# Kernel tuning notes

Measured on AMD Instinct MI355X. Metric: run time of the kernel, lower is better.

## Reference

```python
import jax, jax.numpy as jnp
import numpy as np

NPOINT, RADIUS, SIGMA, K = 1024, 0.1, 0.05, 32
KDE_K = 128  # N_points default of kernel_density_estimation_ball


def setup_inputs() -> dict:
    key = jax.random.key(0)
    ks = jax.random.split(key, 9)
    B, N, C = 4, 4096, 16

    def glorot(k, shape):
        fan_in, fan_out = shape
        return jax.random.normal(k, shape, jnp.float32) * jnp.sqrt(2.0 / (fan_in + fan_out))

    return {
        'xyz': jax.random.uniform(ks[0], (B, N, 3), jnp.float32),      # unit cube
        'feature': jax.random.normal(ks[1], (B, N, C), jnp.float32),
        'w_mlp0': glorot(ks[2], (3 + C, 128)),
        'w_mlp1': glorot(ks[3], (128, 128)),
        'w_mlp2': glorot(ks[4], (128, 256)),
        'w_wn': glorot(ks[5], (3, 32)),
        'w_nl0': glorot(ks[6], (1, 16)),
        'w_nl1': glorot(ks[7], (16, 1)),
        'w_np': glorot(ks[8], (32, 256)),
    }


def _pdist2(a, b):
    # squared pairwise distances [B, M, N]
    return (jnp.sum(a * a, -1)[:, :, None] + jnp.sum(b * b, -1)[:, None, :]
            - 2.0 * jnp.einsum('bmd,bnd->bmn', a, b))


def _fps(xyz, npoint):
    # farthest point sampling, seeded at index 0 (matches CUDA op semantics)
    B, N, _ = xyz.shape

    def step(carry, _):
        min_d, last = carry
        p = jnp.take_along_axis(xyz, last[:, None, None], axis=1)  # [B,1,3]
        d = jnp.sum((xyz - p) ** 2, -1)                            # [B,N]
        min_d = jnp.minimum(min_d, d)
        nxt = jnp.argmax(min_d, axis=1).astype(jnp.int32)
        return (min_d, nxt), nxt

    init = (jnp.full((B, N), jnp.inf, xyz.dtype), jnp.zeros((B,), jnp.int32))
    _, rest = jax.lax.scan(step, init, None, length=npoint - 1)
    return jnp.concatenate([jnp.zeros((B, 1), jnp.int32), rest.T], axis=1)  # [B,npoint]


def _ball_query(xyz, radius, k):
    # first-k-in-index-order neighbors with d2 < r^2, padded with first hit
    B, N, _ = xyz.shape
    d2 = _pdist2(xyz, xyz)
    in_ball = d2 < radius * radius                 # self always included
    j = jnp.arange(N, dtype=jnp.int32)
    keys = jnp.where(in_ball, j, j + N)            # in-ball indices sort first
    _, idx = jax.lax.top_k(-keys, k)               # k smallest keys -> positions j
    cnt = jnp.minimum(jnp.sum(in_ball, axis=-1), k)            # [B,N]
    valid = jnp.arange(k) < cnt[..., None]
    idx = jnp.where(valid, idx, idx[..., :1])
    return idx, cnt


def _kde_ball(xyz, radius, sigma, kde_k):
    idx, cnt = _ball_query(xyz, radius, kde_k)     # [B,N,kde_k], [B,N]
    b_ix = jnp.arange(xyz.shape[0])[:, None, None]
    g = xyz[b_ix, idx] - xyz[:, :, None, :]        # [B,N,kde_k,3]
    R = jnp.sqrt(jnp.float32(sigma))
    quad = jnp.sum(jnp.square(g / R), axis=-1)     # [B,N,kde_k]
    mvn = jnp.exp(-0.5 * quad - 3.0 * jnp.log(R) - 1.5 * jnp.log(2.0 * 3.1415926))
    first = mvn[..., :1]
    total = jnp.sum(mvn, axis=-1, keepdims=True)
    cntf = cnt.astype(xyz.dtype)[..., None]
    total = total - first * (jnp.float32(kde_k) - cntf)  # remove padded duplicates
    return total / cntf                             # [B,N,1]


def _knn(k, src, q):
    d2 = _pdist2(q, src)                            # [B,P,N]
    _, idx = jax.lax.top_k(-d2, k)                  # ascending distance
    return idx


def _forward(xyz, feature, w_mlp0, w_mlp1, w_mlp2, w_wn, w_nl0, w_nl1, w_np):
    B = xyz.shape[0]
    conv = lambda x, w: jax.nn.relu(jnp.einsum('bpkc,cf->bpkf', x, w))  # bias-free 1x1 conv

    fps_idx = _fps(xyz, NPOINT)
    new_xyz = jnp.take_along_axis(xyz, fps_idx[..., None], axis=1)      # [B,P,3]

    knn_idx = _knn(K, xyz, new_xyz)                                      # [B,P,K]
    b_ix = jnp.arange(B)[:, None, None]
    grouped_xyz = xyz[b_ix, knn_idx] - new_xyz[:, :, None, :]            # [B,P,K,3]
    grouped_feature = jnp.concatenate([grouped_xyz, feature[b_ix, knn_idx]], axis=-1)

    inv_density = 1.0 / _kde_ball(xyz, RADIUS, SIGMA, KDE_K)             # [B,N,1]
    grouped_density = inv_density[b_ix, knn_idx]                          # [B,P,K,1]
    density_scale = grouped_density / jnp.max(grouped_density, axis=2, keepdims=True)

    h = conv(conv(conv(grouped_feature, w_mlp0), w_mlp1), w_mlp2)        # [B,P,K,256]
    weight = conv(grouped_xyz, w_wn)                                      # [B,P,K,32]
    density_scale = conv(conv(density_scale, w_nl0), w_nl1)               # [B,P,K,1]

    pts = h * density_scale
    pts = jnp.einsum('bpkc,bpkw->bpcw', pts, weight)                      # [B,P,256,32]
    # np_conv: 1x1 kernel with stride [1, mlp[-1]] + VALID -> only c=0 slice survives
    out = jax.nn.relu(jnp.einsum('bpw,wf->bpf', pts[:, :, 0, :], w_np))   # [B,P,256]
    return new_xyz, out


def reference(xyz, feature, w_mlp0, w_mlp1, w_mlp2, w_wn, w_nl0, w_nl1, w_np):
    return _forward(xyz, feature, w_mlp0, w_mlp1, w_mlp2, w_wn, w_nl0, w_nl1, w_np)
```

## Files before the change

kernel.cpp:

```cpp
#include <hip/hip_runtime.h>
#include <math.h>

#pragma clang fp contract(off)

typedef float v2f __attribute__((ext_vector_type(2)));

__device__ __forceinline__ v2f pk_fma(v2f a, v2f b, v2f c) {
    v2f d;
    asm("v_pk_fma_f32 %0, %1, %2, %3" : "=v"(d) : "v"(a), "v"(b), "v"(c));
    return d;
}

__global__ __launch_bounds__(256) void prep_kernel(
    const float* __restrict__ xyz, const float* __restrict__ w0,
    const float* __restrict__ w1, const float* __restrict__ w2,
    float* __restrict__ norms, float* __restrict__ W1T,
    float* __restrict__ W2c)
{
    int t = blockIdx.x * 256 + threadIdx.x;
    if (t < 16384) {
        float x = xyz[t*3+0], y = xyz[t*3+1], z = xyz[t*3+2];
        norms[t] = (x*x + y*y) + z*z;
        int c = t >> 7, k = t & 127;
        W1T[c*128 + k] = w1[k*128 + c];
    }
    if (t < 128)  { W2c[t] = w2[t*256]; }
}

template<int CTRL>
__device__ __forceinline__ double dpp_f64(double v) {
    int lo = __double2loint(v), hi = __double2hiint(v);
    int plo = __builtin_amdgcn_update_dpp(lo, lo, CTRL, 0xF, 0xF, false);
    int phi = __builtin_amdgcn_update_dpp(hi, hi, CTRL, 0xF, 0xF, false);
    return __hiloint2double(phi, plo);
}
template<int CTRL>
__device__ __forceinline__ double max_f64_dpp(double k) {
    return fmax(dpp_f64<CTRL>(k), k);
}
#define KD(md2bits_f, ipi) __hiloint2double(__float_as_int(md2bits_f), (int)(ipi))

__global__ __launch_bounds__(512) void fps_kde_kernel(
    const float* __restrict__ xyz, const float* __restrict__ norms,
    float* __restrict__ new_xyz, float* __restrict__ invden)
{
    __shared__ float4 pts[4096];
    __shared__ float  nxb[3072];
    __shared__ __attribute__((aligned(16))) double swkd[2][4];
    int tid = threadIdx.x;

    if (blockIdx.x < 4) {
        int b = blockIdx.x;
        const float* Xb = xyz + b*12288;
        for (int t = tid; t < 4096; t += 512)
            pts[t] = make_float4(Xb[t*3+0], Xb[t*3+1], Xb[t*3+2], 0.0f);
        __syncthreads();
        if (tid < 256) {
            int lane = tid & 63, wave = tid >> 6;
            v2f Xp[8], Yp[8], Zp[8], md2[8];
            unsigned ip[16];
#pragma unroll
            for (int k = 0; k < 8; ++k) {
                float4 A = pts[(2*k)*256 + tid];
                float4 B = pts[(2*k+1)*256 + tid];
                Xp[k].x = A.x;  Xp[k].y = B.x;
                Yp[k].x = A.y;  Yp[k].y = B.y;
                Zp[k].x = A.z;  Zp[k].y = B.z;
                md2[k].x = INFINITY; md2[k].y = INFINITY;
                ip[2*k]   = ~((unsigned)((2*k)*256 + tid));
                ip[2*k+1] = ~((unsigned)((2*k+1)*256 + tid));
            }
            float cx = pts[0].x, cy = pts[0].y, cz = pts[0].z;
            if (tid == 0) { nxb[0] = cx; nxb[1] = cy; nxb[2] = cz; }
            int buf = 0;
            for (int it = 1; it < 1024; ++it) {
                v2f cx2, cy2, cz2;
                cx2.x = cx; cx2.y = cx;
                cy2.x = cy; cy2.y = cy;
                cz2.x = cz; cz2.y = cz;
#pragma unroll
                for (int k = 0; k < 8; ++k) {
                    v2f dx = Xp[k] - cx2, dy = Yp[k] - cy2, dz = Zp[k] - cz2;
                    v2f dd = (dx*dx + dy*dy) + dz*dz;
                    md2[k] = __builtin_elementwise_min(md2[k], dd);
                }
                double t0 = fmax(fmax(KD(md2[0].x,ip[0]),  KD(md2[0].y,ip[1])),
                                 fmax(KD(md2[1].x,ip[2]),  KD(md2[1].y,ip[3])));
                double t1 = fmax(fmax(KD(md2[2].x,ip[4]),  KD(md2[2].y,ip[5])),
                                 fmax(KD(md2[3].x,ip[6]),  KD(md2[3].y,ip[7])));
                double t2 = fmax(fmax(KD(md2[4].x,ip[8]),  KD(md2[4].y,ip[9])),
                                 fmax(KD(md2[5].x,ip[10]), KD(md2[5].y,ip[11])));
                double t3 = fmax(fmax(KD(md2[6].x,ip[12]), KD(md2[6].y,ip[13])),
                                 fmax(KD(md2[7].x,ip[14]), KD(md2[7].y,ip[15])));
                double key = fmax(fmax(t0, t1), fmax(t2, t3));
                key = max_f64_dpp<0xB1>(key);
                key = max_f64_dpp<0x4E>(key);
                key = max_f64_dpp<0x141>(key);
                key = max_f64_dpp<0x140>(key);
                key = max_f64_dpp<0x142>(key);
                key = max_f64_dpp<0x143>(key);
                if (lane == 63) swkd[buf][wave] = key;
                __syncthreads();
                double2 wab = *((const double2*)&swkd[buf][0]);
                double2 wcd = *((const double2*)&swkd[buf][2]);
                double kk = fmax(fmax(wab.x, wab.y), fmax(wcd.x, wcd.y));
                int fp = (int)(~((unsigned)__double2loint(kk)));
                float4 c = pts[fp];
                cx = c.x; cy = c.y; cz = c.z;
                if (tid == 0) { nxb[it*3+0] = cx; nxb[it*3+1] = cy; nxb[it*3+2] = cz; }
                buf ^= 1;
            }
        } else {
            for (int it = 1; it < 1024; ++it) __syncthreads();
        }
        __syncthreads();
        float* NX = new_xyz + b*3072;
        for (int t = tid; t < 3072; t += 512) NX[t] = nxb[t];
    } else {
        int idx = blockIdx.x - 4;
        int b = idx >> 9;
        int wave = tid >> 6, lane = tid & 63;
        int i_local = ((idx & 511) << 3) + wave;
        const float* Xb = xyz + b*12288;
        const float* Nb = norms + b*4096;
        for (int t = tid; t < 4096; t += 512)
            pts[t] = make_float4(Xb[t*3+0], Xb[t*3+1], Xb[t*3+2], Nb[t]);
        __syncthreads();
        float4 c = pts[i_local];
        const float Rv    = sqrtf(0.05f);
        const float inv_s = 1.0f / (Rv*Rv);
        const float K1    = -3.0f*logf(Rv) - 1.5f*logf(2.0f*3.1415926f);
        float csum = 0.0f; int cnt = 0;
        for (int j = lane; j < 4096; j += 64) {
            float4 q = pts[j];
            float dot = (c.x*q.x + c.y*q.y) + c.z*q.z;
            float t2 = 2.0f * dot;
            float d2 = (c.w + q.w) - t2;
            if (d2 < 0.01f) {
                float gx = q.x - c.x, gy = q.y - c.y, gz = q.z - c.z;
                float dd = (gx*gx + gy*gy) + gz*gz;
                csum += expf(-0.5f * (dd * inv_s) + K1);
                cnt  += 1;
            }
        }
#pragma unroll
        for (int m = 1; m < 64; m <<= 1) {
            csum += __shfl_xor(csum, m, 64);
            cnt  += __shfl_xor(cnt,  m, 64);
        }
        if (lane == 0) {
            float den = csum / (float)cnt;
            invden[b*4096 + i_local] = 1.0f / den;
        }
    }
}

__global__ __launch_bounds__(256) void knn_kernel(
    const float* __restrict__ xyz, const float* __restrict__ norms,
    const float* __restrict__ new_xyz, int* __restrict__ knn_idx)
{
    __shared__ unsigned sd2[4*4096];
    __shared__ int sIdx[4*32];
    int wave = threadIdx.x >> 6, lane = threadIdx.x & 63;
    int qg = blockIdx.x*4 + wave;
    int b = qg >> 10;
    const float* Q = new_xyz + qg*3;
    float qx = Q[0], qy = Q[1], qz = Q[2];
    float nq = (qx*qx + qy*qy) + qz*qz;
    const float* Xb = xyz + b*12288;
    const float* Nb = norms + b*4096;
    unsigned* d2w = sd2 + wave*4096;
    for (int j = lane; j < 4096; j += 64) {
        float x = Xb[j*3+0], y = Xb[j*3+1], z = Xb[j*3+2];
        float dot = (qx*x + qy*y) + qz*z;
        float t2 = 2.0f*dot;
        float d = (nq + Nb[j]) - t2;
        unsigned u = __float_as_uint(d);
        unsigned m = ((unsigned)((int)u >> 31)) | 0x80000000u;
        d2w[j] = u ^ m;
    }
    for (int r = 0; r < 32; ++r) {
        double a0 = -INFINITY, a1 = -INFINITY, a2 = -INFINITY, a3 = -INFINITY;
#pragma unroll
        for (int t = 0; t < 16; ++t) {
            int jb = t*256 + lane*4;
            uint4 v = *((const uint4*)(d2w + jb));
            a0 = fmax(a0, __hiloint2double((int)v.x, jb));
            a1 = fmax(a1, __hiloint2double((int)v.y, jb+1));
            a2 = fmax(a2, __hiloint2double((int)v.z, jb+2));
            a3 = fmax(a3, __hiloint2double((int)v.w, jb+3));
        }
        double key = fmax(fmax(a0, a1), fmax(a2, a3));
        key = max_f64_dpp<0xB1>(key);
        key = max_f64_dpp<0x4E>(key);
        key = max_f64_dpp<0x141>(key);
        key = max_f64_dpp<0x140>(key);
        key = max_f64_dpp<0x142>(key);
        key = max_f64_dpp<0x143>(key);
        int jwin = __builtin_amdgcn_readlane(__double2loint(key), 63);
        if (lane == 0) { sIdx[wave*32 + r] = jwin; d2w[jwin] = 0xFFFFFFFFu; }
    }
    if (lane < 32) knn_idx[qg*32 + lane] = sIdx[wave*32 + lane];
}

__global__ __launch_bounds__(256, 2) void group_mlp_kernel(
    const float* __restrict__ xyz, const float* __restrict__ feat,
    const float* __restrict__ new_xyz, const int* __restrict__ knn_idx,
    const float* __restrict__ invden,
    const float* __restrict__ w0, const float* __restrict__ W1T,
    const float* __restrict__ W2c, const float* __restrict__ wwn,
    const float* __restrict__ wnl0, const float* __restrict__ wnl1,
    float* __restrict__ ptsw)
{
    __shared__ float sW1[16384];
    {
        const float4* g4 = (const float4*)W1T;
        float4* s4 = (float4*)sW1;
#pragma unroll
        for (int i = 0; i < 16; ++i)
            s4[i*256 + threadIdx.x] = g4[i*256 + threadIdx.x];
    }

    int row = blockIdx.x*256 + threadIdx.x;
    int k  = row & 31;
    int pg = row >> 5;
    int b  = row >> 15;
    int j  = knn_idx[row];
    const float* Xb = xyz + b*12288;
    const float* Q  = new_xyz + pg*3;
    float in[19];
    in[0] = Xb[j*3+0] - Q[0];
    in[1] = Xb[j*3+1] - Q[1];
    in[2] = Xb[j*3+2] - Q[2];
    const float4* F = (const float4*)(feat + (size_t)(b*4096 + j)*16);
    float4 f0 = F[0], f1 = F[1], f2 = F[2], f3 = F[3];
    in[3]=f0.x; in[4]=f0.y; in[5]=f0.z; in[6]=f0.w;
    in[7]=f1.x; in[8]=f1.y; in[9]=f1.z; in[10]=f1.w;
    in[11]=f2.x; in[12]=f2.y; in[13]=f2.z; in[14]=f2.w;
    in[15]=f3.x; in[16]=f3.y; in[17]=f3.z; in[18]=f3.w;

    float gd = invden[b*4096 + j];
    float mx = gd;
#pragma unroll
    for (int m = 1; m < 32; m <<= 1) mx = fmaxf(mx, __shfl_xor(mx, m, 64));
    float dsc = gd / mx;
    float sacc = 0.0f;
#pragma unroll
    for (int t = 0; t < 16; ++t)
        sacc = fmaf(fmaxf(dsc * wnl0[t], 0.0f), wnl1[t], sacc);
    float ds = fmaxf(sacc, 0.0f);

    v2f h1v[64];
    const v2f* W0v = (const v2f*)w0;
#pragma unroll
    for (int cc = 0; cc < 64; ++cc) {
        v2f in0; in0.x = in[0]; in0.y = in[0];
        v2f acc = in0 * W0v[cc];
#pragma unroll
        for (int i = 1; i < 19; ++i) {
            v2f ini; ini.x = in[i]; ini.y = in[i];
            acc = pk_fma(ini, W0v[i*64 + cc], acc);
        }
        v2f z; z.x = 0.0f; z.y = 0.0f;
        h1v[cc] = __builtin_elementwise_max(acc, z);
    }
    __syncthreads();

    float acc0 = 0.0f;
    for (int c2 = 0; c2 < 128; ++c2) {
        const float4* w4 = (const float4*)(sW1 + c2*128);
        v2f a01; a01.x = 0.0f; a01.y = 0.0f;
        v2f a23; a23.x = 0.0f; a23.y = 0.0f;
#pragma unroll
        for (int kk = 0; kk < 32; ++kk) {
            float4 wv = w4[kk];
            v2f wab; wab.x = wv.x; wab.y = wv.y;
            v2f wcd; wcd.x = wv.z; wcd.y = wv.w;
            a01 = pk_fma(h1v[2*kk],   wab, a01);
            a23 = pk_fma(h1v[2*kk+1], wcd, a23);
        }
        float a = (a01.x + a01.y) + (a23.x + a23.y);
        acc0 = fmaf(fmaxf(a, 0.0f), W2c[c2], acc0);
    }
    float h0 = fmaxf(acc0, 0.0f);
    float s = h0 * ds;

    float gx = in[0], gy = in[1], gz = in[2];
    float* pw = ptsw + pg*32;
#pragma unroll
    for (int w = 0; w < 32; ++w) {
        float a = gx * wwn[w];
        a = fmaf(gy, wwn[32+w], a);
        a = fmaf(gz, wwn[64+w], a);
        float part = s * fmaxf(a, 0.0f);
#pragma unroll
        for (int m = 1; m < 32; m <<= 1) part += __shfl_xor(part, m, 64);
        if (k == 0) pw[w] = part;
    }
}

__global__ __launch_bounds__(256) void final_kernel(
    const float* __restrict__ ptsw, const float* __restrict__ wnp,
    float* __restrict__ out)
{
    int pg = blockIdx.x;
    int f  = threadIdx.x;
    const float* pw = ptsw + pg*32;
    float a = 0.0f;
#pragma unroll
    for (int w = 0; w < 32; ++w) a = fmaf(pw[w], wnp[w*256+f], a);
    out[pg*256 + f] = fmaxf(a, 0.0f);
}

extern "C" void kernel_launch(void* const* d_in, const int* in_sizes, int n_in,
                              void* d_out, int out_size, void* d_ws, size_t ws_size,
                              hipStream_t stream) {
    const float* xyz  = (const float*)d_in[0];
    const float* feat = (const float*)d_in[1];
    const float* w0   = (const float*)d_in[2];
    const float* w1   = (const float*)d_in[3];
    const float* w2   = (const float*)d_in[4];
    const float* wwn  = (const float*)d_in[5];
    const float* wnl0 = (const float*)d_in[6];
    const float* wnl1 = (const float*)d_in[7];
    const float* wnp  = (const float*)d_in[8];

    float* out_all  = (float*)d_out;
    float* new_xyz  = out_all;
    float* out2     = out_all + 12288;

    char* ws = (char*)d_ws;
    float* norms  = (float*)(ws + 0);
    float* invden = (float*)(ws + 65536);
    int*   knn    = (int*)  (ws + 131072);
    float* ptsw   = (float*)(ws + 655360);
    float* W1T    = (float*)(ws + 1189376);
    float* W2c    = (float*)(ws + 1254912);

    prep_kernel<<<64, 256, 0, stream>>>(xyz, w0, w1, w2, norms, W1T, W2c);
    fps_kde_kernel<<<2052, 512, 0, stream>>>(xyz, norms, new_xyz, invden);
    knn_kernel<<<1024, 256, 0, stream>>>(xyz, norms, new_xyz, knn);
    group_mlp_kernel<<<512, 256, 0, stream>>>(xyz, feat, new_xyz, knn, invden,
                                              w0, W1T, W2c, wwn, wnl0, wnl1,
                                              ptsw);
    final_kernel<<<4096, 256, 0, stream>>>(ptsw, wnp, out2);
}
```

Before: 796.5 us.

## Fuse kNN into FPS kernel with beacon-based streaming of sampled points

```diff
diff --git a/kernel.cpp b/kernel.cpp
--- a/kernel.cpp
+++ b/kernel.cpp
@@ -15,9 +15,10 @@
     const float* __restrict__ xyz, const float* __restrict__ w0,
     const float* __restrict__ w1, const float* __restrict__ w2,
     float* __restrict__ norms, float* __restrict__ W1T,
-    float* __restrict__ W2c)
+    float* __restrict__ W2c, unsigned* __restrict__ flags)
 {
     int t = blockIdx.x * 256 + threadIdx.x;
+    if (t < 8) flags[t] = 0u;
     if (t < 16384) {
         float x = xyz[t*3+0], y = xyz[t*3+1], z = xyz[t*3+2];
         norms[t] = (x*x + y*y) + z*z;
@@ -42,16 +43,19 @@
 
 __global__ __launch_bounds__(512) void fps_kde_kernel(
     const float* __restrict__ xyz, const float* __restrict__ norms,
-    float* __restrict__ new_xyz, float* __restrict__ invden)
+    float* __restrict__ new_xyz, float* __restrict__ invden,
+    int* __restrict__ knn_idx, unsigned* __restrict__ flags)
 {
     __shared__ float4 pts[4096];
-    __shared__ float  nxb[3072];
     __shared__ __attribute__((aligned(16))) double swkd[2][4];
+    __shared__ int sIdxS[4][32];
     int tid = threadIdx.x;
+    unsigned* beacon = flags + 4;
 
     if (blockIdx.x < 4) {
         int b = blockIdx.x;
         const float* Xb = xyz + b*12288;
+        float* NX = new_xyz + b*3072;
         for (int t = tid; t < 4096; t += 512)
             pts[t] = make_float4(Xb[t*3+0], Xb[t*3+1], Xb[t*3+2], 0.0f);
         __syncthreads();
@@ -71,7 +75,7 @@
                 ip[2*k+1] = ~((unsigned)((2*k+1)*256 + tid));
             }
             float cx = pts[0].x, cy = pts[0].y, cz = pts[0].z;
-            if (tid == 0) { nxb[0] = cx; nxb[1] = cy; nxb[2] = cz; }
+            if (tid == 0) { NX[0] = cx; NX[1] = cy; NX[2] = cz; }
             int buf = 0;
             for (int it = 1; it < 1024; ++it) {
                 v2f cx2, cy2, cz2;
@@ -107,16 +111,22 @@
                 int fp = (int)(~((unsigned)__double2loint(kk)));
                 float4 c = pts[fp];
                 cx = c.x; cy = c.y; cz = c.z;
-                if (tid == 0) { nxb[it*3+0] = cx; nxb[it*3+1] = cy; nxb[it*3+2] = cz; }
+                if (tid == 0) {
+                    NX[it*3+0] = cx; NX[it*3+1] = cy; NX[it*3+2] = cz;
+                    if ((it & 31) == 31)
+                        __hip_atomic_store(beacon + b, (unsigned)(it + 1),
+                                           __ATOMIC_RELEASE,
+                                           __HIP_MEMORY_SCOPE_AGENT);
+                }
                 buf ^= 1;
             }
+            if (tid == 0)
+                __hip_atomic_store(beacon + b, 1024u, __ATOMIC_RELEASE,
+                                   __HIP_MEMORY_SCOPE_AGENT);
         } else {
             for (int it = 1; it < 1024; ++it) __syncthreads();
         }
-        __syncthreads();
-        float* NX = new_xyz + b*3072;
-        for (int t = tid; t < 3072; t += 512) NX[t] = nxb[t];
-    } else {
+    } else if (blockIdx.x < 2052) {
         int idx = blockIdx.x - 4;
         int b = idx >> 9;
         int wave = tid >> 6, lane = tid & 63;
@@ -152,55 +162,55 @@
             float den = csum / (float)cnt;
             invden[b*4096 + i_local] = 1.0f / den;
         }
-    }
-}
-
-__global__ __launch_bounds__(256) void knn_kernel(
-    const float* __restrict__ xyz, const float* __restrict__ norms,
-    const float* __restrict__ new_xyz, int* __restrict__ knn_idx)
-{
-    __shared__ unsigned sd2[4*4096];
-    __shared__ int sIdx[4*32];
-    int wave = threadIdx.x >> 6, lane = threadIdx.x & 63;
-    int qg = blockIdx.x*4 + wave;
-    int b = qg >> 10;
-    const float* Q = new_xyz + qg*3;
-    float qx = Q[0], qy = Q[1], qz = Q[2];
-    float nq = (qx*qx + qy*qy) + qz*qz;
-    const float* Xb = xyz + b*12288;
-    const float* Nb = norms + b*4096;
-    unsigned* d2w = sd2 + wave*4096;
-    for (int j = lane; j < 4096; j += 64) {
-        float x = Xb[j*3+0], y = Xb[j*3+1], z = Xb[j*3+2];
-        float dot = (qx*x + qy*y) + qz*z;
-        float t2 = 2.0f*dot;
-        float d = (nq + Nb[j]) - t2;
-        unsigned u = __float_as_uint(d);
-        unsigned m = ((unsigned)((int)u >> 31)) | 0x80000000u;
-        d2w[j] = u ^ m;
-    }
-    for (int r = 0; r < 32; ++r) {
-        double a0 = -INFINITY, a1 = -INFINITY, a2 = -INFINITY, a3 = -INFINITY;
-#pragma unroll
-        for (int t = 0; t < 16; ++t) {
-            int jb = t*256 + lane*4;
-            uint4 v = *((const uint4*)(d2w + jb));
-            a0 = fmax(a0, __hiloint2double((int)v.x, jb));
-            a1 = fmax(a1, __hiloint2double((int)v.y, jb+1));
-            a2 = fmax(a2, __hiloint2double((int)v.z, jb+2));
-            a3 = fmax(a3, __hiloint2double((int)v.w, jb+3));
-        }
-        double key = fmax(fmax(a0, a1), fmax(a2, a3));
-        key = max_f64_dpp<0xB1>(key);
-        key = max_f64_dpp<0x4E>(key);
-        key = max_f64_dpp<0x141>(key);
-        key = max_f64_dpp<0x140>(key);
-        key = max_f64_dpp<0x142>(key);
-        key = max_f64_dpp<0x143>(key);
-        int jwin = __builtin_amdgcn_readlane(__double2loint(key), 63);
-        if (lane == 0) { sIdx[wave*32 + r] = jwin; d2w[jwin] = 0xFFFFFFFFu; }
-    }
-    if (lane < 32) knn_idx[qg*32 + lane] = sIdx[wave*32 + lane];
+    } else {
+        int wave = tid >> 6, lane = tid & 63;
+        if (wave >= 4) return;
+        int cc = blockIdx.x - 2052;
+        int qg = cc*4 + wave;
+        int b2 = qg >> 10;
+        int q  = qg & 1023;
+        while (__hip_atomic_load(beacon + b2, __ATOMIC_ACQUIRE,
+                                 __HIP_MEMORY_SCOPE_AGENT) <= (unsigned)q)
+            __builtin_amdgcn_s_sleep(64);
+        const float* Q = new_xyz + qg*3;
+        float qx = Q[0], qy = Q[1], qz = Q[2];
+        float nq = (qx*qx + qy*qy) + qz*qz;
+        const float* Xb = xyz + b2*12288;
+        const float* Nb = norms + b2*4096;
+        unsigned* d2w = ((unsigned*)pts) + wave*4096;
+        for (int j = lane; j < 4096; j += 64) {
+            float x = Xb[j*3+0], y = Xb[j*3+1], z = Xb[j*3+2];
+            float dot = (qx*x + qy*y) + qz*z;
+            float t2 = 2.0f*dot;
+            float d = (nq + Nb[j]) - t2;
+            unsigned u = __float_as_uint(d);
+            unsigned m = ((unsigned)((int)u >> 31)) | 0x80000000u;
+            d2w[j] = u ^ m;
+        }
+        for (int r = 0; r < 32; ++r) {
+            double a0 = -INFINITY, a1 = -INFINITY,
+                   a2 = -INFINITY, a3 = -INFINITY;
+#pragma unroll
+            for (int t = 0; t < 16; ++t) {
+                int jb = t*256 + lane*4;
+                uint4 v = *((const uint4*)(d2w + jb));
+                a0 = fmax(a0, __hiloint2double((int)v.x, jb));
+                a1 = fmax(a1, __hiloint2double((int)v.y, jb+1));
+                a2 = fmax(a2, __hiloint2double((int)v.z, jb+2));
+                a3 = fmax(a3, __hiloint2double((int)v.w, jb+3));
+            }
+            double key = fmax(fmax(a0, a1), fmax(a2, a3));
+            key = max_f64_dpp<0xB1>(key);
+            key = max_f64_dpp<0x4E>(key);
+            key = max_f64_dpp<0x141>(key);
+            key = max_f64_dpp<0x140>(key);
+            key = max_f64_dpp<0x142>(key);
+            key = max_f64_dpp<0x143>(key);
+            int jwin = __builtin_amdgcn_readlane(__double2loint(key), 63);
+            if (lane == 0) { sIdxS[wave][r] = jwin; d2w[jwin] = 0xFFFFFFFFu; }
+        }
+        if (lane < 32) knn_idx[qg*32 + lane] = sIdxS[wave][lane];
+    }
 }
 
 __global__ __launch_bounds__(256, 2) void group_mlp_kernel(
@@ -336,10 +346,12 @@
     float* ptsw   = (float*)(ws + 655360);
     float* W1T    = (float*)(ws + 1189376);
     float* W2c    = (float*)(ws + 1254912);
-
-    prep_kernel<<<64, 256, 0, stream>>>(xyz, w0, w1, w2, norms, W1T, W2c);
-    fps_kde_kernel<<<2052, 512, 0, stream>>>(xyz, norms, new_xyz, invden);
-    knn_kernel<<<1024, 256, 0, stream>>>(xyz, norms, new_xyz, knn);
+    unsigned* flags = (unsigned*)(ws + 1255424);
+
+    prep_kernel<<<64, 256, 0, stream>>>(xyz, w0, w1, w2, norms, W1T, W2c,
+                                        flags);
+    fps_kde_kernel<<<3076, 512, 0, stream>>>(xyz, norms, new_xyz, invden,
+                                             knn, flags);
     group_mlp_kernel<<<512, 256, 0, stream>>>(xyz, feat, new_xyz, knn, invden,
                                               w0, W1T, W2c, wwn, wnl0, wnl1,
                                               ptsw);
```

Result: slower. 819.4 us (+2.9%).
